# Performance work log

Hardware: AMD Instinct MI355X
Metric: run time of the kernel (lower is better)

## Reference

```python
import jax, jax.numpy as jnp
import numpy as np

E = 1024          # n_embed_dim
H = 64            # head_size = n_embed_dim // n_heads (16)

def setup_inputs() -> dict:
    key = jax.random.key(0)
    k_x, k_q, k_k, k_v = jax.random.split(key, 4)
    scale = 1.0 / np.sqrt(E)
    return {
        "x": jax.random.normal(k_x, (4, 2048, E), dtype=jnp.float32),
        "ln_gamma": jnp.ones((E,), jnp.float32),
        "ln_beta": jnp.zeros((E,), jnp.float32),
        # torch nn.Linear weights: [out_features, in_features]
        "Wq": jax.random.normal(k_q, (H, E), dtype=jnp.float32) * scale,
        "Wk": jax.random.normal(k_k, (H, E), dtype=jnp.float32) * scale,
        "Wv": jax.random.normal(k_v, (H, E), dtype=jnp.float32) * scale,
    }

def reference(x, ln_gamma, ln_beta, Wq, Wk, Wv):
    # LayerNorm over last dim (eps matches torch default 1e-5)
    mu = jnp.mean(x, axis=-1, keepdims=True)
    var = jnp.mean(jnp.square(x - mu), axis=-1, keepdims=True)
    xn = (x - mu) * jax.lax.rsqrt(var + 1e-5) * ln_gamma + ln_beta

    q = jnp.einsum('bse,he->bsh', xn, Wq)   # [B,S,H]
    k = jnp.einsum('bse,he->bsh', xn, Wk)
    v = jnp.einsum('bse,he->bsh', xn, Wv)

    scores = jnp.einsum('bqh,bkh->bqk', q, k) / jnp.sqrt(jnp.float32(H))
    S = x.shape[1]
    causal = jnp.tril(jnp.ones((S, S), dtype=bool))
    scores = jnp.where(causal, scores, -jnp.inf)
    attn = jax.nn.softmax(scores, axis=-1)
    return jnp.einsum('bqk,bkh->bqh', attn, v)
```

## Files before the change

### kernel.cpp

```cpp
#include <hip/hip_runtime.h>

#define E 1024
#define HH 64
#define BB 4
#define SS 2048
#define BS (BB*SS)
#define NSLOT 144

typedef unsigned short u16;
typedef short bf16x8 __attribute__((ext_vector_type(8)));
typedef float f32x4 __attribute__((ext_vector_type(4)));

#define LOG2E_O8 0.18033688011112042f

__device__ inline u16 f2bf(float f) {
    unsigned int u = __float_as_uint(f);
    unsigned int r = (u + 0x7FFFu + ((u >> 16) & 1u)) >> 16;
    return (u16)r;
}
__device__ inline float bf2f(u16 h) {
    return __uint_as_float(((unsigned int)h) << 16);
}
__device__ inline unsigned int pk2(float lo, float hi) {
    return (unsigned int)f2bf(lo) | ((unsigned int)f2bf(hi) << 16);
}

__global__ __launch_bounds__(256, 1) void lnqkv(const float* __restrict__ x,
        const float* __restrict__ gamma, const float* __restrict__ beta,
        const float* __restrict__ Wq, const float* __restrict__ Wk,
        const float* __restrict__ Wv,
        u16* __restrict__ qb, u16* __restrict__ kb, u16* __restrict__ vt) {
    const int mb   = blockIdx.x >> 1;
    const int half = blockIdx.x & 1;
    const int row0 = mb * 32;
    const int t = threadIdx.x;
    const int w = t >> 6, lane = t & 63;
    const int quad = lane >> 4, r15 = lane & 15;
    const int mt = w >> 1, cgrp = w & 1;
    __shared__ u16 Xs[8 * 32 * 128];
    __shared__ u16 Ws[2][96 * 128];
    f32x4 acc[3] = {};
    const int xrow = mt * 16 + r15;

    {
        const float4* gr = (const float4*)gamma;
        const float4* br = (const float4*)beta;
        float4 g[4], bt[4];
        #pragma unroll
        for (int i = 0; i < 4; ++i) { g[i] = gr[lane + 64 * i]; bt[i] = br[lane + 64 * i]; }
        #pragma unroll
        for (int rb = 0; rb < 2; ++rb) {
            float4 v[4][4];
            #pragma unroll
            for (int rr = 0; rr < 4; ++rr) {
                const int row = w * 8 + rb * 4 + rr;
                const float4* xr = (const float4*)(x + (size_t)(row0 + row) * E);
                #pragma unroll
                for (int i = 0; i < 4; ++i) v[rr][i] = xr[lane + 64 * i];
            }
            #pragma unroll
            for (int rr = 0; rr < 4; ++rr) {
                const int row = w * 8 + rb * 4 + rr;
                float s = 0.f, sq = 0.f;
                #pragma unroll
                for (int i = 0; i < 4; ++i) {
                    s  += v[rr][i].x + v[rr][i].y + v[rr][i].z + v[rr][i].w;
                    sq += v[rr][i].x*v[rr][i].x + v[rr][i].y*v[rr][i].y
                        + v[rr][i].z*v[rr][i].z + v[rr][i].w*v[rr][i].w;
                }
                #pragma unroll
                for (int off = 32; off > 0; off >>= 1) {
                    s  += __shfl_xor(s,  off);
                    sq += __shfl_xor(sq, off);
                }
                const float mean = s * (1.0f / E);
                const float var  = sq * (1.0f / E) - mean * mean;
                const float rstd = rsqrtf(var + 1e-5f);
                #pragma unroll
                for (int i = 0; i < 4; ++i) {
                    ushort4 o;
                    o.x = f2bf((v[rr][i].x - mean) * rstd * g[i].x + bt[i].x);
                    o.y = f2bf((v[rr][i].y - mean) * rstd * g[i].y + bt[i].y);
                    o.z = f2bf((v[rr][i].z - mean) * rstd * g[i].z + bt[i].z);
                    o.w = f2bf((v[rr][i].w - mean) * rstd * g[i].w + bt[i].w);
                    const int p = lane + 64 * i;
                    const int dst = (p >> 5) * 4096 + row * 128 + ((p >> 4) & 1) * 64
                                  + ((((p >> 1) & 7) ^ (row & 7)) * 8) + (p & 1) * 4;
                    *(ushort4*)&Xs[dst] = o;
                }
            }
        }
    }

    auto stageW = [&](int kc, int buf) {
        #pragma unroll
        for (int i = 0; i < 6; ++i) {
            const int idx = i * 256 + t;
            const int wl = idx >> 4, u = idx & 15;
            const int hf = u >> 3, ch = u & 7;
            const int grow = half * 96 + wl;
            const float* src = (grow < 64)  ? (Wq + (size_t)grow * E)
                             : (grow < 128) ? (Wk + (size_t)(grow - 64) * E)
                                            : (Wv + (size_t)(grow - 128) * E);
            const float4 a  = *(const float4*)(src + kc * 128 + u * 8);
            const float4 b2 = *(const float4*)(src + kc * 128 + u * 8 + 4);
            uint4 d;
            d.x = pk2(a.x,  a.y);  d.y = pk2(a.z,  a.w);
            d.z = pk2(b2.x, b2.y); d.w = pk2(b2.z, b2.w);
            *(uint4*)&Ws[buf][wl * 128 + hf * 64 + (ch ^ (wl & 7)) * 8] = d;
        }
    };

    stageW(0, 0);
    __syncthreads();

    for (int kc8 = 0; kc8 < 8; ++kc8) {
        const int cur = kc8 & 1;
        if (kc8 < 7) stageW(kc8 + 1, cur ^ 1);
        const u16* Xc = &Xs[kc8 * 4096];
        #pragma unroll
        for (int kk = 0; kk < 4; ++kk) {
            const int hf = kk >> 1, q4 = (kk & 1) * 4 + quad;
            const bf16x8 af = *(const bf16x8*)&Xc[xrow * 128 + hf * 64 + (q4 ^ (xrow & 7)) * 8];
            #pragma unroll
            for (int j = 0; j < 3; ++j) {
                const int wl = (cgrp * 3 + j) * 16 + r15;
                const bf16x8 bfr = *(const bf16x8*)&Ws[cur][wl * 128 + hf * 64 + (q4 ^ (wl & 7)) * 8];
                acc[j] = __builtin_amdgcn_mfma_f32_16x16x32_bf16(af, bfr, acc[j], 0, 0, 0);
            }
        }
        __syncthreads();
    }

    const int b    = row0 >> 11;
    const int key0 = row0 & 2047;
    #pragma unroll
    for (int j = 0; j < 3; ++j) {
        const int cg  = half * 96 + cgrp * 48 + j * 16 + r15;
        const int sel = cg >> 6;
        const int col = cg & 63;
        if (sel < 2) {
            u16* base = (sel == 0) ? qb : kb;
            const float esc = (sel == 0) ? LOG2E_O8 : 1.0f;
            #pragma unroll
            for (int r = 0; r < 4; ++r) {
                const size_t row = (size_t)row0 + mt * 16 + quad * 4 + r;
                base[row * HH + col] = f2bf(acc[j][r] * esc);
            }
        } else {
            ushort4 pk;
            pk.x = f2bf(acc[j][0]); pk.y = f2bf(acc[j][1]);
            pk.z = f2bf(acc[j][2]); pk.w = f2bf(acc[j][3]);
            *(ushort4*)(vt + (size_t)b * HH * SS + (size_t)col * SS
                           + key0 + mt * 16 + quad * 4) = pk;
        }
    }
}

__global__ __launch_bounds__(256) void attn_partial(const u16* __restrict__ qb,
        const u16* __restrict__ kb, const u16* __restrict__ vt,
        u16* __restrict__ po, float* __restrict__ pl,
        float* __restrict__ out) {
    const int bid = blockIdx.x;
    const int b   = bid / 72;
    const int s2  = bid - b * 72;
    int a = (int)((sqrtf(4.0f * s2 + 1.0f) - 1.0f) * 0.5f);
    while ((a + 1) * (a + 2) <= s2) ++a;
    while (a * (a + 1) > s2) --a;
    const int rem = s2 - a * (a + 1);
    const int rp  = rem / (a + 1);
    const int c   = rem - rp * (a + 1);
    const int qt0 = 4 * a + 2 * rp;
    const int nc  = a + 1;
    const int t = threadIdx.x;
    const int w = t >> 6, lane = t & 63;
    const int quad = lane >> 4, r15 = lane & 15;

    __shared__ u16 Ks[4 * 64 * 64];
    __shared__ u16 VT[4 * 64 * 64];
    __shared__ u16 Ps[64 * 64];

    bf16x8 qf0[2], qf1[2];
    #pragma unroll
    for (int qi = 0; qi < 2; ++qi) {
        const size_t qrow = ((size_t)b * SS + (qt0 + qi) * 64 + w * 16 + r15) * HH;
        qf0[qi] = *(const bf16x8*)(qb + qrow + quad * 8);
        qf1[qi] = *(const bf16x8*)(qb + qrow + 32 + quad * 8);
    }

    const int ntmax = (c < a) ? 4 : (2 * rp + 2);

    {
        const int row = t >> 2, ch0 = (t & 3) * 2;
        for (int tl = 0; tl < ntmax; ++tl) {
            const int kt = (c * 4 + tl) << 6;
            const uint4* srcK = (const uint4*)(kb + ((size_t)b * SS + kt + row) * HH + ch0 * 8);
            const uint4 k0 = srcK[0], k1 = srcK[1];
            *(uint4*)&Ks[tl * 4096 + row * 64 + ((ch0    ) ^ (row & 7)) * 8] = k0;
            *(uint4*)&Ks[tl * 4096 + row * 64 + ((ch0 + 1) ^ (row & 7)) * 8] = k1;
            const uint4* srcV = (const uint4*)(vt + (size_t)b * HH * SS + (size_t)row * SS
                                               + kt + ch0 * 8);
            const uint4 v0 = srcV[0], v1 = srcV[1];
            *(uint4*)&VT[tl * 4096 + row * 64 + ((ch0    ) ^ (row & 7)) * 8] = v0;
            *(uint4*)&VT[tl * 4096 + row * 64 + ((ch0 + 1) ^ (row & 7)) * 8] = v1;
        }
    }
    __syncthreads();

    f32x4 o[2][4] = {};
    float l_[2][4] = {};

    for (int tl = 0; tl < ntmax; ++tl) {
        const int tile = c * 4 + tl;
        const u16* KsT = &Ks[tl * 4096];
        const u16* VTT = &VT[tl * 4096];

        bf16x8 kf0[4], kf1[4], vf0[4], vf1[4];
        #pragma unroll
        for (int nt = 0; nt < 4; ++nt) {
            const int krow = nt * 16 + r15;
            kf0[nt] = *(const bf16x8*)&KsT[krow * 64 + ((    quad) ^ (krow & 7)) * 8];
            kf1[nt] = *(const bf16x8*)&KsT[krow * 64 + ((4 + quad) ^ (krow & 7)) * 8];
            vf0[nt] = *(const bf16x8*)&VTT[krow * 64 + ((    quad) ^ (krow & 7)) * 8];
            vf1[nt] = *(const bf16x8*)&VTT[krow * 64 + ((4 + quad) ^ (krow & 7)) * 8];
        }

        #pragma unroll
        for (int qi = 0; qi < 2; ++qi) {
            const int qt_i = qt0 + qi;
            if (tile > qt_i) continue;

            f32x4 s4[4] = {};
            #pragma unroll
            for (int nt = 0; nt < 4; ++nt) {
                s4[nt] = __builtin_amdgcn_mfma_f32_16x16x32_bf16(qf0[qi], kf0[nt], s4[nt], 0, 0, 0);
                s4[nt] = __builtin_amdgcn_mfma_f32_16x16x32_bf16(qf1[qi], kf1[nt], s4[nt], 0, 0, 0);
            }
            if (tile == qt_i) {
                #pragma unroll
                for (int nt = 0; nt < 4; ++nt)
                    #pragma unroll
                    for (int r = 0; r < 4; ++r)
                        if (nt * 16 + r15 > w * 16 + quad * 4 + r) s4[nt][r] = -INFINITY;
            }

            float p[4][4];
            #pragma unroll
            for (int r = 0; r < 4; ++r) {
                #pragma unroll
                for (int nt = 0; nt < 4; ++nt)
                    p[nt][r] = __builtin_amdgcn_exp2f(s4[nt][r]);
                l_[qi][r] += (p[0][r] + p[1][r]) + (p[2][r] + p[3][r]);
            }

            #pragma unroll
            for (int nt = 0; nt < 4; ++nt)
                #pragma unroll
                for (int r = 0; r < 4; ++r) {
                    const int prow = w * 16 + quad * 4 + r;
                    const int col  = nt * 16 + r15;
                    Ps[prow * 64 + (((col >> 3) ^ (prow & 7)) * 8) + (col & 7)] = f2bf(p[nt][r]);
                }
            const int arow = w * 16 + r15;
            const bf16x8 pf0 = *(const bf16x8*)&Ps[arow * 64 + ((    quad) ^ (arow & 7)) * 8];
            const bf16x8 pf1 = *(const bf16x8*)&Ps[arow * 64 + ((4 + quad) ^ (arow & 7)) * 8];

            #pragma unroll
            for (int ht = 0; ht < 4; ++ht) {
                o[qi][ht] = __builtin_amdgcn_mfma_f32_16x16x32_bf16(pf0, vf0[ht], o[qi][ht], 0, 0, 0);
                o[qi][ht] = __builtin_amdgcn_mfma_f32_16x16x32_bf16(pf1, vf1[ht], o[qi][ht], 0, 0, 0);
            }
        }
    }

    #pragma unroll
    for (int qi = 0; qi < 2; ++qi)
        #pragma unroll
        for (int r = 0; r < 4; ++r) {
            l_[qi][r] += __shfl_xor(l_[qi][r], 1); l_[qi][r] += __shfl_xor(l_[qi][r], 2);
            l_[qi][r] += __shfl_xor(l_[qi][r], 4); l_[qi][r] += __shfl_xor(l_[qi][r], 8);
        }

    #pragma unroll
    for (int qi = 0; qi < 2; ++qi) {
        const int qt_i = qt0 + qi;
        if (nc == 1) {
            #pragma unroll
            for (int r = 0; r < 4; ++r) {
                const float inv = 1.0f / l_[qi][r];
                const size_t orow = ((size_t)b * SS + qt_i * 64 + w * 16 + quad * 4 + r) * HH;
                #pragma unroll
                for (int ht = 0; ht < 4; ++ht)
                    out[orow + ht * 16 + r15] = o[qi][ht][r] * inv;
            }
        } else {
            const int slot = b * NSLOT + 2 * a * (a + 1) + (2 * rp + qi) * (a + 1) + c;
            #pragma unroll
            for (int r = 0; r < 4; ++r) {
                const int q = w * 16 + quad * 4 + r;
                #pragma unroll
                for (int ht = 0; ht < 4; ++ht)
                    po[(size_t)slot * 4096 + q * 64 + ht * 16 + r15] = f2bf(o[qi][ht][r]);
                if (r15 == 0) pl[slot * 64 + q] = l_[qi][r];
            }
        }
    }
}

__global__ __launch_bounds__(256) void attn_reduce(const u16* __restrict__ po,
        const float* __restrict__ pl, float* __restrict__ out) {
    const int bid = blockIdx.x;
    const int b = bid / 112, rem = bid - b * 112;
    const int qt = 4 + (rem >> 2), qq = rem & 3;
    const int a = qt >> 2, r_ = qt & 3;
    const int nc = a + 1;
    const int sbase = b * NSLOT + 2 * a * (a + 1) + r_ * (a + 1);
    const int t = threadIdx.x;
    const int h = t & 63, qr = t >> 6;
    #pragma unroll
    for (int i = 0; i < 4; ++i) {
        const int q = qq * 16 + qr * 4 + i;
        float osum = 0.f, lsum = 0.f;
        #pragma unroll
        for (int cidx = 0; cidx < 8; ++cidx) {
            if (cidx < nc) {
                osum += bf2f(po[(size_t)(sbase + cidx) * 4096 + q * 64 + h]);
                lsum += pl[(sbase + cidx) * 64 + q];
            }
        }
        out[((size_t)b * SS + (qt << 6) + q) * HH + h] = osum / lsum;
    }
}

extern "C" void kernel_launch(void* const* d_in, const int* in_sizes, int n_in,
                              void* d_out, int out_size, void* d_ws, size_t ws_size,
                              hipStream_t stream) {
    const float* x     = (const float*)d_in[0];
    const float* gamma = (const float*)d_in[1];
    const float* beta  = (const float*)d_in[2];
    const float* Wq    = (const float*)d_in[3];
    const float* Wk    = (const float*)d_in[4];
    const float* Wv    = (const float*)d_in[5];
    float* out = (float*)d_out;

    char* p = (char*)d_ws;
    u16*   qb   = (u16*)p;                         p += (size_t)BS * HH * 2;
    u16*   kb   = (u16*)p;                         p += (size_t)BS * HH * 2;
    u16*   vt   = (u16*)p;                         p += (size_t)BS * HH * 2;
    u16*   po   = (u16*)p;                         p += (size_t)BB * NSLOT * 4096 * 2;
    float* pl   = (float*)p;

    lnqkv       <<<BS / 16,  256, 0, stream>>>(x, gamma, beta, Wq, Wk, Wv, qb, kb, vt);
    attn_partial<<<BB * 72,  256, 0, stream>>>(qb, kb, vt, po, pl, out);
    attn_reduce <<<BB * 112, 256, 0, stream>>>(po, pl, out);
}
```

Before: 133.7 us.

## Shrink LDS in lnqkv by keeping normalized X in registers, double-buffer per chunk

The LayerNorm stage now has each thread own one row and an 8-element column slice. The normalized bf16 values are held in 16 uint4 registers, and only the current and next 128-column chunks go into a double-buffered LDS tile instead of the full 32x1024 tile. This shrinks shared memory from 64KB-plus to 32KB-plus, so launch bounds can ask for two blocks per CU. It also swaps the software bf16 rounding for the hardware v_cvt_pk_bf16_f32 instruction. The costs are x being read twice from global memory (or cache), gamma and beta loads per thread, and higher register pressure from the su array.

Result: slower. 138.4 us (+3.5%).

```diff
diff --git a/kernel.cpp b/kernel.cpp
--- a/kernel.cpp
+++ b/kernel.cpp
@@ -21,11 +21,13 @@
 __device__ inline float bf2f(u16 h) {
     return __uint_as_float(((unsigned int)h) << 16);
 }
-__device__ inline unsigned int pk2(float lo, float hi) {
-    return (unsigned int)f2bf(lo) | ((unsigned int)f2bf(hi) << 16);
-}
-
-__global__ __launch_bounds__(256, 1) void lnqkv(const float* __restrict__ x,
+__device__ inline unsigned int cvtpk(float lo, float hi) {
+    unsigned int r;
+    asm("v_cvt_pk_bf16_f32 %0, %1, %2" : "=v"(r) : "v"(lo), "v"(hi));
+    return r;
+}
+
+__global__ __launch_bounds__(256, 2) void lnqkv(const float* __restrict__ x,
         const float* __restrict__ gamma, const float* __restrict__ beta,
         const float* __restrict__ Wq, const float* __restrict__ Wk,
         const float* __restrict__ Wv,
@@ -37,67 +39,62 @@
     const int w = t >> 6, lane = t & 63;
     const int quad = lane >> 4, r15 = lane & 15;
     const int mt = w >> 1, cgrp = w & 1;
-    __shared__ u16 Xs[8 * 32 * 128];
+    __shared__ u16 Xs[2][32 * 128];
     __shared__ u16 Ws[2][96 * 128];
     f32x4 acc[3] = {};
     const int xrow = mt * 16 + r15;
 
-    {
-        const float4* gr = (const float4*)gamma;
-        const float4* br = (const float4*)beta;
-        float4 g[4], bt[4];
-        #pragma unroll
-        for (int i = 0; i < 4; ++i) { g[i] = gr[lane + 64 * i]; bt[i] = br[lane + 64 * i]; }
-        #pragma unroll
-        for (int rb = 0; rb < 2; ++rb) {
-            float4 v[4][4];
-            #pragma unroll
-            for (int rr = 0; rr < 4; ++rr) {
-                const int row = w * 8 + rb * 4 + rr;
-                const float4* xr = (const float4*)(x + (size_t)(row0 + row) * E);
-                #pragma unroll
-                for (int i = 0; i < 4; ++i) v[rr][i] = xr[lane + 64 * i];
-            }
-            #pragma unroll
-            for (int rr = 0; rr < 4; ++rr) {
-                const int row = w * 8 + rb * 4 + rr;
-                float s = 0.f, sq = 0.f;
-                #pragma unroll
-                for (int i = 0; i < 4; ++i) {
-                    s  += v[rr][i].x + v[rr][i].y + v[rr][i].z + v[rr][i].w;
-                    sq += v[rr][i].x*v[rr][i].x + v[rr][i].y*v[rr][i].y
-                        + v[rr][i].z*v[rr][i].z + v[rr][i].w*v[rr][i].w;
-                }
-                #pragma unroll
-                for (int off = 32; off > 0; off >>= 1) {
-                    s  += __shfl_xor(s,  off);
-                    sq += __shfl_xor(sq, off);
-                }
-                const float mean = s * (1.0f / E);
-                const float var  = sq * (1.0f / E) - mean * mean;
-                const float rstd = rsqrtf(var + 1e-5f);
-                #pragma unroll
-                for (int i = 0; i < 4; ++i) {
-                    ushort4 o;
-                    o.x = f2bf((v[rr][i].x - mean) * rstd * g[i].x + bt[i].x);
-                    o.y = f2bf((v[rr][i].y - mean) * rstd * g[i].y + bt[i].y);
-                    o.z = f2bf((v[rr][i].z - mean) * rstd * g[i].z + bt[i].z);
-                    o.w = f2bf((v[rr][i].w - mean) * rstd * g[i].w + bt[i].w);
-                    const int p = lane + 64 * i;
-                    const int dst = (p >> 5) * 4096 + row * 128 + ((p >> 4) & 1) * 64
-                                  + ((((p >> 1) & 7) ^ (row & 7)) * 8) + (p & 1) * 4;
-                    *(ushort4*)&Xs[dst] = o;
-                }
-            }
-        }
-    }
+    const int row = t >> 3, ch = t & 7;
+    const float* xrp = x + (size_t)(row0 + row) * E + ch * 8;
+
+    float s = 0.f, sq = 0.f;
+    #pragma unroll
+    for (int g16 = 0; g16 < 16; ++g16) {
+        const int off = (g16 >> 1) * 128 + (g16 & 1) * 64;
+        const float4 a  = *(const float4*)(xrp + off);
+        const float4 b2 = *(const float4*)(xrp + off + 4);
+        s  += (a.x + a.y) + (a.z + a.w) + (b2.x + b2.y) + (b2.z + b2.w);
+        sq += a.x*a.x + a.y*a.y + a.z*a.z + a.w*a.w
+            + b2.x*b2.x + b2.y*b2.y + b2.z*b2.z + b2.w*b2.w;
+    }
+    s  += __shfl_xor(s, 1);  sq += __shfl_xor(sq, 1);
+    s  += __shfl_xor(s, 2);  sq += __shfl_xor(sq, 2);
+    s  += __shfl_xor(s, 4);  sq += __shfl_xor(sq, 4);
+    const float mean = s * (1.0f / E);
+    const float var  = sq * (1.0f / E) - mean * mean;
+    const float rstd = rsqrtf(var + 1e-5f);
+
+    uint4 su[16];
+    #pragma unroll
+    for (int g16 = 0; g16 < 16; ++g16) {
+        const int off = (g16 >> 1) * 128 + (g16 & 1) * 64;
+        const float4 a  = *(const float4*)(xrp + off);
+        const float4 b2 = *(const float4*)(xrp + off + 4);
+        const float4 g0 = *(const float4*)(gamma + ch * 8 + off);
+        const float4 g1 = *(const float4*)(gamma + ch * 8 + off + 4);
+        const float4 t0 = *(const float4*)(beta  + ch * 8 + off);
+        const float4 t1 = *(const float4*)(beta  + ch * 8 + off + 4);
+        const float e0 = (a.x  - mean) * rstd * g0.x + t0.x;
+        const float e1 = (a.y  - mean) * rstd * g0.y + t0.y;
+        const float e2 = (a.z  - mean) * rstd * g0.z + t0.z;
+        const float e3 = (a.w  - mean) * rstd * g0.w + t0.w;
+        const float e4 = (b2.x - mean) * rstd * g1.x + t1.x;
+        const float e5 = (b2.y - mean) * rstd * g1.y + t1.y;
+        const float e6 = (b2.z - mean) * rstd * g1.z + t1.z;
+        const float e7 = (b2.w - mean) * rstd * g1.w + t1.w;
+        su[g16].x = cvtpk(e0, e1); su[g16].y = cvtpk(e2, e3);
+        su[g16].z = cvtpk(e4, e5); su[g16].w = cvtpk(e6, e7);
+    }
+
+    const int xdst0 = row * 128 +  0 + ((ch ^ (row & 7)) * 8);
+    const int xdst1 = row * 128 + 64 + ((ch ^ (row & 7)) * 8);
 
     auto stageW = [&](int kc, int buf) {
         #pragma unroll
         for (int i = 0; i < 6; ++i) {
             const int idx = i * 256 + t;
             const int wl = idx >> 4, u = idx & 15;
-            const int hf = u >> 3, ch = u & 7;
+            const int hf = u >> 3, ch2 = u & 7;
             const int grow = half * 96 + wl;
             const float* src = (grow < 64)  ? (Wq + (size_t)grow * E)
                              : (grow < 128) ? (Wk + (size_t)(grow - 64) * E)
@@ -105,23 +102,30 @@
             const float4 a  = *(const float4*)(src + kc * 128 + u * 8);
             const float4 b2 = *(const float4*)(src + kc * 128 + u * 8 + 4);
             uint4 d;
-            d.x = pk2(a.x,  a.y);  d.y = pk2(a.z,  a.w);
-            d.z = pk2(b2.x, b2.y); d.w = pk2(b2.z, b2.w);
-            *(uint4*)&Ws[buf][wl * 128 + hf * 64 + (ch ^ (wl & 7)) * 8] = d;
+            d.x = cvtpk(a.x,  a.y);  d.y = cvtpk(a.z,  a.w);
+            d.z = cvtpk(b2.x, b2.y); d.w = cvtpk(b2.z, b2.w);
+            *(uint4*)&Ws[buf][wl * 128 + hf * 64 + (ch2 ^ (wl & 7)) * 8] = d;
         }
     };
 
+    *(uint4*)&Xs[0][xdst0] = su[0];
+    *(uint4*)&Xs[0][xdst1] = su[1];
     stageW(0, 0);
     __syncthreads();
 
+    #pragma unroll
     for (int kc8 = 0; kc8 < 8; ++kc8) {
         const int cur = kc8 & 1;
-        if (kc8 < 7) stageW(kc8 + 1, cur ^ 1);
-        const u16* Xc = &Xs[kc8 * 4096];
+        if (kc8 < 7) {
+            const int nxt = cur ^ 1;
+            *(uint4*)&Xs[nxt][xdst0] = su[(kc8 + 1) * 2 + 0];
+            *(uint4*)&Xs[nxt][xdst1] = su[(kc8 + 1) * 2 + 1];
+            stageW(kc8 + 1, nxt);
+        }
         #pragma unroll
         for (int kk = 0; kk < 4; ++kk) {
             const int hf = kk >> 1, q4 = (kk & 1) * 4 + quad;
-            const bf16x8 af = *(const bf16x8*)&Xc[xrow * 128 + hf * 64 + (q4 ^ (xrow & 7)) * 8];
+            const bf16x8 af = *(const bf16x8*)&Xs[cur][xrow * 128 + hf * 64 + (q4 ^ (xrow & 7)) * 8];
             #pragma unroll
             for (int j = 0; j < 3; ++j) {
                 const int wl = (cgrp * 3 + j) * 16 + r15;
@@ -144,8 +148,8 @@
             const float esc = (sel == 0) ? LOG2E_O8 : 1.0f;
             #pragma unroll
             for (int r = 0; r < 4; ++r) {
-                const size_t row = (size_t)row0 + mt * 16 + quad * 4 + r;
-                base[row * HH + col] = f2bf(acc[j][r] * esc);
+                const size_t orow = (size_t)row0 + mt * 16 + quad * 4 + r;
+                base[orow * HH + col] = f2bf(acc[j][r] * esc);
             }
         } else {
             ushort4 pk;
```
